# Optimization experiments

Hardware: AMD Instinct MI355X
Metric: run time of the kernel (lower is better)

The kernel has to match this reference:

```python
import jax, jax.numpy as jnp
import numpy as np
import math

N_HEAD = 12

def _tiled_causal_mask(T):
    # t x t lower-triangular mask tiled 3x3 -> T x T (T divisible by 3)
    t = T // 3
    tril = jnp.tril(jnp.ones((t, t), dtype=bool))
    return jnp.tile(tril, (3, 3))  # [T, T]

def setup_inputs() -> dict:
    key = jax.random.key(0)
    ks = jax.random.split(key, 5)
    B, T, C = 4, 1536, 768
    s = 1.0 / math.sqrt(C)
    return {
        "x": jax.random.normal(ks[0], (B, T, C), dtype=jnp.float32),
        "Wq": jax.random.normal(ks[1], (C, C), dtype=jnp.float32) * s,
        "bq": jnp.zeros((C,), dtype=jnp.float32),
        "Wk": jax.random.normal(ks[2], (C, C), dtype=jnp.float32) * s,
        "bk": jnp.zeros((C,), dtype=jnp.float32),
        "Wv": jax.random.normal(ks[3], (C, C), dtype=jnp.float32) * s,
        "bv": jnp.zeros((C,), dtype=jnp.float32),
        "Wp": jax.random.normal(ks[4], (C, C), dtype=jnp.float32) * s,
        "bp": jnp.zeros((C,), dtype=jnp.float32),
    }

def reference(x, Wq, bq, Wk, bk, Wv, bv, Wp, bp):
    B, T, C = x.shape
    H = N_HEAD
    D = C // H  # head dim
    def heads(W, b):
        return (x @ W.T + b).reshape(B, T, H, D).transpose(0, 2, 1, 3)  # [B,H,T,D]
    q = heads(Wq, bq)
    k = heads(Wk, bk)
    v = heads(Wv, bv)
    att = jnp.einsum('bhqd,bhkd->bhqk', q, k) * (1.0 / math.sqrt(D))  # [B,H,T,T]
    mask = _tiled_causal_mask(T)  # [T,T] bool
    att = jnp.where(mask[None, None], att, jnp.float32(-jnp.inf))
    att = jax.nn.softmax(att, axis=-1)
    y = jnp.einsum('bhqk,bhkd->bhqd', att, v)  # [B,H,T,D]
    y = y.transpose(0, 2, 1, 3).reshape(B, T, C)
    return y @ Wp.T + bp
```

## Files before the change

### kernel.cpp

```cpp
#include <hip/hip_runtime.h>
#include <hip/hip_bf16.h>

typedef __attribute__((ext_vector_type(8))) short bf16x8;
typedef __attribute__((ext_vector_type(4))) float f32x4;

#define NH 12
#define HD 64
#define TT 1536
#define CC 768
#define BB 4
#define MM (BB * TT)
#define LOG2E 1.44269504088896f
#define SSHIFT 14.4269504089f

__device__ __forceinline__ unsigned short f2bf(float f) {
    unsigned int u = __builtin_bit_cast(unsigned int, f);
    return (unsigned short)((u + 0x7FFFu + ((u >> 16) & 1u)) >> 16);
}

__device__ __forceinline__ unsigned short nbf(float f) {
    __hip_bfloat16 h = __float2bfloat16(f);
    return __builtin_bit_cast(unsigned short, h);
}

__device__ __forceinline__ void gl_lds16(const unsigned short* g, unsigned short* l) {
    __builtin_amdgcn_global_load_lds(
        (const __attribute__((address_space(1))) void*)g,
        (__attribute__((address_space(3))) void*)l,
        16, 0, 0);
}

#define N4W (CC * CC / 4)
#define N4X (MM * CC / 4)
__global__ __launch_bounds__(256) void convert_all(
    const float* __restrict__ x,
    const float* __restrict__ w0, const float* __restrict__ w1,
    const float* __restrict__ w2, const float* __restrict__ w3,
    unsigned short* __restrict__ xo,
    unsigned short* __restrict__ o0, unsigned short* __restrict__ o1,
    unsigned short* __restrict__ o2, unsigned short* __restrict__ o3) {
    int i = blockIdx.x * 256 + threadIdx.x;
    const float* in;
    unsigned short* out;
    int j;
    if (i < N4X) {
        in = x; out = xo; j = i;
    } else {
        int t = i - N4X;
        int which = t / N4W;
        j = t - which * N4W;
        in = which == 0 ? w0 : which == 1 ? w1 : which == 2 ? w2 : w3;
        out = which == 0 ? o0 : which == 1 ? o1 : which == 2 ? o2 : o3;
    }
    float4 v = reinterpret_cast<const float4*>(in)[j];
    ushort4 o = { f2bf(v.x), f2bf(v.y), f2bf(v.z), f2bf(v.w) };
    reinterpret_cast<ushort4*>(out)[j] = o;
}

#define GEMM_KLOOP(APTR, BPTR)                                                \
    for (int kt = 0; kt < 12; kt++) {                                         \
        const int k0 = kt * 64;                                               \
        __syncthreads();                                                      \
        _Pragma("unroll")                                                     \
        for (int i = 0; i < 4; i++) {                                         \
            gl_lds16(&APTR[(size_t)(m0 + i * 32 + sr) * CC + k0 + sc],        \
                     as0 + (i * 32 + w * 8) * 64);                            \
            gl_lds16(&BPTR[(size_t)(n0 + i * 32 + sr) * CC + k0 + sc],        \
                     bs0 + (i * 32 + w * 8) * 64);                            \
        }                                                                     \
        __syncthreads();                                                      \
        _Pragma("unroll")                                                     \
        for (int s = 0; s < 2; s++) {                                         \
            const int swz = ((s * 4 + fg) ^ (fr & 7)) * 8;                    \
            bf16x8 a[4], b[4];                                                \
            _Pragma("unroll")                                                 \
            for (int mi = 0; mi < 4; mi++)                                    \
                a[mi] = *reinterpret_cast<const bf16x8*>(                     \
                    as0 + (wr * 64 + mi * 16 + fr) * 64 + swz);               \
            _Pragma("unroll")                                                 \
            for (int ni = 0; ni < 4; ni++)                                    \
                b[ni] = *reinterpret_cast<const bf16x8*>(                     \
                    bs0 + (wc * 64 + ni * 16 + fr) * 64 + swz);               \
            _Pragma("unroll")                                                 \
            for (int mi = 0; mi < 4; mi++)                                    \
                _Pragma("unroll")                                             \
                for (int ni = 0; ni < 4; ni++)                                \
                    acc[mi][ni] = __builtin_amdgcn_mfma_f32_16x16x32_bf16(    \
                        a[mi], b[ni], acc[mi][ni], 0, 0, 0);                  \
        }                                                                     \
    }

__global__ __launch_bounds__(256) void gemm_qkv(
    const unsigned short* __restrict__ xb,
    const unsigned short* __restrict__ wq, const float* __restrict__ bq,
    const unsigned short* __restrict__ wk, const float* __restrict__ bk,
    const unsigned short* __restrict__ wv, const float* __restrict__ bv,
    unsigned short* __restrict__ qo, unsigned short* __restrict__ ko,
    unsigned short* __restrict__ vo) {
    __shared__ unsigned short As[128][64];
    __shared__ unsigned short Bs[128][64];

    const int wg = (blockIdx.x & 7) * 108 + (blockIdx.x >> 3);
    const int z = wg / 288;
    const int rem = wg % 288;
    const int m0 = (rem / 6) * 128;
    const int n0 = (rem % 6) * 128;

    const unsigned short* W = (z == 0) ? wq : (z == 1) ? wk : wv;
    const float* bias = (z == 0) ? bq : (z == 1) ? bk : bv;
    unsigned short* out = (z == 0) ? qo : (z == 1) ? ko : vo;
    const float scale = (z == 0) ? 0.125f * LOG2E : 1.0f;

    const int tid = threadIdx.x;
    const int lane = tid & 63;
    const int w = tid >> 6;
    const int wr = w >> 1, wc = w & 1;
    const int fr = lane & 15, fg = lane >> 4;

    const int sr = tid >> 3;
    const int sc = ((tid & 7) ^ ((tid >> 3) & 7)) * 8;
    unsigned short* as0 = &As[0][0];
    unsigned short* bs0 = &Bs[0][0];

    f32x4 acc[4][4];
#pragma unroll
    for (int ni = 0; ni < 4; ni++) {
        float bv_ = bias[n0 + wc * 64 + ni * 16 + fr];
#pragma unroll
        for (int mi = 0; mi < 4; mi++)
            acc[mi][ni] = (f32x4){bv_, bv_, bv_, bv_};
    }

    GEMM_KLOOP(xb, W)

#pragma unroll
    for (int mi = 0; mi < 4; mi++)
#pragma unroll
        for (int ni = 0; ni < 4; ni++) {
            int n = n0 + wc * 64 + ni * 16 + fr;
            int h = n >> 6, d = n & 63;
            int m_base = m0 + wr * 64 + mi * 16 + fg * 4;
            int b_ = m_base / TT, t0 = m_base % TT;
            if (z == 2) {
                size_t off = ((size_t)(b_ * NH + h) * HD + d) * (size_t)TT + t0;
                ushort4 o = { nbf(acc[mi][ni][0]), nbf(acc[mi][ni][1]),
                              nbf(acc[mi][ni][2]), nbf(acc[mi][ni][3]) };
                *reinterpret_cast<ushort4*>(&out[off]) = o;
            } else {
#pragma unroll
                for (int r = 0; r < 4; r++) {
                    size_t off = ((size_t)(b_ * NH + h) * TT + t0 + r) * (size_t)HD + d;
                    out[off] = nbf(acc[mi][ni][r] * scale);
                }
            }
        }
}

__global__ __launch_bounds__(256) void gemm_proj(
    const unsigned short* __restrict__ yb,
    const unsigned short* __restrict__ wp, const float* __restrict__ bp,
    float* __restrict__ out) {
    __shared__ unsigned short As[128][64];
    __shared__ unsigned short Bs[128][64];

    const int wg = (blockIdx.x & 7) * 36 + (blockIdx.x >> 3);
    const int m0 = (wg / 6) * 128;
    const int n0 = (wg % 6) * 128;

    const int tid = threadIdx.x;
    const int lane = tid & 63;
    const int w = tid >> 6;
    const int wr = w >> 1, wc = w & 1;
    const int fr = lane & 15, fg = lane >> 4;

    const int sr = tid >> 3;
    const int sc = ((tid & 7) ^ ((tid >> 3) & 7)) * 8;
    unsigned short* as0 = &As[0][0];
    unsigned short* bs0 = &Bs[0][0];

    f32x4 acc[4][4];
#pragma unroll
    for (int ni = 0; ni < 4; ni++) {
        float bv_ = bp[n0 + wc * 64 + ni * 16 + fr];
#pragma unroll
        for (int mi = 0; mi < 4; mi++)
            acc[mi][ni] = (f32x4){bv_, bv_, bv_, bv_};
    }

    GEMM_KLOOP(yb, wp)

#pragma unroll
    for (int mi = 0; mi < 4; mi++)
#pragma unroll
        for (int ni = 0; ni < 4; ni++) {
            int n = n0 + wc * 64 + ni * 16 + fr;
#pragma unroll
            for (int r = 0; r < 4; r++) {
                int m = m0 + wr * 64 + mi * 16 + fg * 4 + r;
                out[(size_t)m * CC + n] = acc[mi][ni][r];
            }
        }
}

__global__ __launch_bounds__(128, 4) void attn(
    const unsigned short* __restrict__ q, const unsigned short* __restrict__ k,
    const unsigned short* __restrict__ vt, unsigned short* __restrict__ y) {
    __shared__ unsigned short Ks[2][32][64];
    __shared__ unsigned short Vs[2][64][32];
    __shared__ unsigned short Ps[2][16][40];

    const int gid = blockIdx.x;
    const int slot = gid & 7;
    const int rest = gid >> 3;
    const int bh = slot * 6 + rest % 6;
    const int rank = rest / 6;
    const int p32 = 15 - rank / 3;
    const int sg0 = rank % 3;
    const int q0 = sg0 * 512 + p32 * 32;

    const int tid = threadIdx.x;
    const int w = tid >> 6;
    const int lane = tid & 63;
    const int fr = lane & 15, fg = lane >> 4;

    const size_t base = (size_t)bh * TT * HD;
    const unsigned short* kk = k + base;
    const unsigned short* vv = vt + base;

    bf16x8 aq[2];
#pragma unroll
    for (int s = 0; s < 2; s++)
        aq[s] = *reinterpret_cast<const bf16x8*>(
            &q[base + (size_t)(q0 + w * 16 + fr) * HD + s * 32 + fg * 8]);

    f32x4 acc_o[4];
#pragma unroll
    for (int i = 0; i < 4; i++) acc_o[i] = (f32x4){0.f, 0.f, 0.f, 0.f};
    f32x4 acc_l = (f32x4){0.f, 0.f, 0.f, 0.f};

    const bf16x8 ones8 = {(short)0x3F80, (short)0x3F80, (short)0x3F80, (short)0x3F80,
                          (short)0x3F80, (short)0x3F80, (short)0x3F80, (short)0x3F80};
    const f32x4 sinit = {-SSHIFT, -SSHIFT, -SSHIFT, -SSHIFT};

    auto stage = [&](int b, int k0n) {
#pragma unroll
        for (int i = 0; i < 2; i++) {
            const int rK = w * 16 + i * 8 + (lane >> 3);
            gl_lds16(&kk[(size_t)(k0n + rK) * HD + (((lane & 7) ^ (rK & 7)) * 8)],
                     &Ks[b][w * 16 + i * 8][0]);
            const int rV = w * 32 + i * 16 + (lane >> 2);
            gl_lds16(&vv[(size_t)rV * TT + k0n + (((lane & 3) ^ (rV & 3)) * 8)],
                     &Vs[b][w * 32 + i * 16][0]);
        }
    };

    const int per = p32 + 1;
    const int ntot = 3 * per;

    stage(0, 0);
    int cur = 0;
    int j = 0;
    int ji = 0, si = 0;
    __syncthreads();

    for (int ci = 0; ci < ntot; ci++) {
        if (ci + 1 < ntot) {
            ji++; if (ji == per) { ji = 0; si++; }
            stage(cur ^ 1, si * 512 + ji * 32);
        }

        f32x4 S[2];
#pragma unroll
        for (int nb = 0; nb < 2; nb++) {
            f32x4 sa = sinit;
            const int krow = nb * 16 + fr;
#pragma unroll
            for (int s = 0; s < 2; s++) {
                bf16x8 bk_ = *reinterpret_cast<const bf16x8*>(
                    &Ks[cur][krow][(((s * 4 + fg) ^ (krow & 7))) * 8]);
                sa = __builtin_amdgcn_mfma_f32_16x16x32_bf16(aq[s], bk_, sa, 0, 0, 0);
            }
            S[nb] = sa;
        }

        if (j == per - 1) {
#pragma unroll
            for (int nb = 0; nb < 2; nb++)
#pragma unroll
                for (int r = 0; r < 4; r++) {
                    int ib = w * 16 + fg * 4 + r;
                    int jb = nb * 16 + fr;
                    if (jb > ib) S[nb][r] = -1e30f;
                }
        }

#pragma unroll
        for (int nb = 0; nb < 2; nb++)
#pragma unroll
            for (int r = 0; r < 4; r++)
                Ps[w][fg * 4 + r][((nb ^ (fg >> 1)) * 16) + fr] =
                    nbf(exp2f(S[nb][r]));

        bf16x8 ap = *reinterpret_cast<const bf16x8*>(
            &Ps[w][fr][(fg ^ (2 * (fr >> 3))) * 8]);
#pragma unroll
        for (int nd = 0; nd < 4; nd++) {
            const int vrow = nd * 16 + fr;
            bf16x8 bv_ = *reinterpret_cast<const bf16x8*>(
                &Vs[cur][vrow][((fg ^ (vrow & 3))) * 8]);
            acc_o[nd] = __builtin_amdgcn_mfma_f32_16x16x32_bf16(ap, bv_, acc_o[nd], 0, 0, 0);
        }
        acc_l = __builtin_amdgcn_mfma_f32_16x16x32_bf16(ap, ones8, acc_l, 0, 0, 0);

        __syncthreads();
        cur ^= 1;
        if (++j == per) j = 0;
    }

    const int b_ = bh / NH, h = bh % NH;
#pragma unroll
    for (int r = 0; r < 4; r++) {
        float inv = 1.f / acc_l[r];
        int t = q0 + w * 16 + fg * 4 + r;
        size_t off = ((size_t)b_ * TT + t) * CC + h * HD;
#pragma unroll
        for (int nd = 0; nd < 4; nd++)
            y[off + nd * 16 + fr] = nbf(acc_o[nd][r] * inv);
    }
}

extern "C" void kernel_launch(void* const* d_in, const int* in_sizes, int n_in,
                              void* d_out, int out_size, void* d_ws, size_t ws_size,
                              hipStream_t stream) {
    const float* x  = (const float*)d_in[0];
    const float* Wq = (const float*)d_in[1];
    const float* bq = (const float*)d_in[2];
    const float* Wk = (const float*)d_in[3];
    const float* bk = (const float*)d_in[4];
    const float* Wv = (const float*)d_in[5];
    const float* bv = (const float*)d_in[6];
    const float* Wp = (const float*)d_in[7];
    const float* bp = (const float*)d_in[8];
    float* out = (float*)d_out;

    unsigned short* ws  = (unsigned short*)d_ws;
    unsigned short* wqb = ws;
    unsigned short* wkb = wqb + (size_t)CC * CC;
    unsigned short* wvb = wkb + (size_t)CC * CC;
    unsigned short* wpb = wvb + (size_t)CC * CC;
    unsigned short* xb  = wpb + (size_t)CC * CC;
    unsigned short* qb_ = xb  + (size_t)MM * CC;
    unsigned short* kb_ = qb_ + (size_t)MM * CC;
    unsigned short* vt_ = kb_ + (size_t)MM * CC;
    unsigned short* yb  = vt_ + (size_t)MM * CC;

    const int ntot4 = N4X + 4 * N4W;
    convert_all<<<(ntot4 + 255) / 256, 256, 0, stream>>>(
        x, Wq, Wk, Wv, Wp, xb, wqb, wkb, wvb, wpb);

    gemm_qkv<<<dim3(864), 256, 0, stream>>>(
        xb, wqb, bq, wkb, bk, wvb, bv, qb_, kb_, vt_);
    attn<<<dim3(2304), 128, 0, stream>>>(qb_, kb_, vt_, yb);
    gemm_proj<<<dim3(288), 256, 0, stream>>>(yb, wpb, bp, out);
}
```

Baseline: 112.1 us.

## Triple-buffer K/V tiles and software-pipeline QK^T one tile ahead in attention

The attention loop now keeps three K/V LDS buffers instead of two, so staging runs two tiles ahead. The QK^T MFMAs for the next tile are issued right after the exp/P write of the current tile, letting them overlap with the softmax and PV work. This is meant to hide global-to-LDS latency and MFMA dependency stalls. In exchange it uses more LDS per block and more live registers for the second S tile, which may lower occupancy under launch_bounds(128,4).

Result: slower. 120.3 us (+7.3%).

```diff
diff --git a/kernel.cpp b/kernel.cpp
--- a/kernel.cpp
+++ b/kernel.cpp
@@ -205,8 +205,8 @@
 __global__ __launch_bounds__(128, 4) void attn(
     const unsigned short* __restrict__ q, const unsigned short* __restrict__ k,
     const unsigned short* __restrict__ vt, unsigned short* __restrict__ y) {
-    __shared__ unsigned short Ks[2][32][64];
-    __shared__ unsigned short Vs[2][64][32];
+    __shared__ unsigned short Ks[3][32][64];
+    __shared__ unsigned short Vs[3][64][32];
     __shared__ unsigned short Ps[2][16][40];
 
     const int gid = blockIdx.x;
@@ -254,22 +254,7 @@
         }
     };
 
-    const int per = p32 + 1;
-    const int ntot = 3 * per;
-
-    stage(0, 0);
-    int cur = 0;
-    int j = 0;
-    int ji = 0, si = 0;
-    __syncthreads();
-
-    for (int ci = 0; ci < ntot; ci++) {
-        if (ci + 1 < ntot) {
-            ji++; if (ji == per) { ji = 0; si++; }
-            stage(cur ^ 1, si * 512 + ji * 32);
-        }
-
-        f32x4 S[2];
+    auto qk = [&](int b, bool dg, f32x4* S) {
 #pragma unroll
         for (int nb = 0; nb < 2; nb++) {
             f32x4 sa = sinit;
@@ -277,21 +262,42 @@
 #pragma unroll
             for (int s = 0; s < 2; s++) {
                 bf16x8 bk_ = *reinterpret_cast<const bf16x8*>(
-                    &Ks[cur][krow][(((s * 4 + fg) ^ (krow & 7))) * 8]);
+                    &Ks[b][krow][(((s * 4 + fg) ^ (krow & 7))) * 8]);
                 sa = __builtin_amdgcn_mfma_f32_16x16x32_bf16(aq[s], bk_, sa, 0, 0, 0);
             }
-            S[nb] = sa;
-        }
-
-        if (j == per - 1) {
-#pragma unroll
-            for (int nb = 0; nb < 2; nb++)
+            if (dg) {
 #pragma unroll
                 for (int r = 0; r < 4; r++) {
                     int ib = w * 16 + fg * 4 + r;
                     int jb = nb * 16 + fr;
-                    if (jb > ib) S[nb][r] = -1e30f;
+                    if (jb > ib) sa[r] = -1e30f;
                 }
+            }
+            S[nb] = sa;
+        }
+    };
+
+    const int per = p32 + 1;
+    const int ntot = 3 * per;
+
+    stage(0, 0);
+    int ji = 0, si = 0;
+    if (ntot > 1) {
+        ji++; if (ji == per) { ji = 0; si++; }
+        stage(1, si * 512 + ji * 32);
+    }
+    __syncthreads();
+
+    int jn = 0;
+    f32x4 S_cur[2];
+    qk(0, jn == per - 1, S_cur);
+
+    int bC = 0, bN = 1, bW = 2;
+
+    for (int ci = 0; ci < ntot; ci++) {
+        if (ci + 2 < ntot) {
+            ji++; if (ji == per) { ji = 0; si++; }
+            stage(bW, si * 512 + ji * 32);
         }
 
 #pragma unroll
@@ -299,7 +305,13 @@
 #pragma unroll
             for (int r = 0; r < 4; r++)
                 Ps[w][fg * 4 + r][((nb ^ (fg >> 1)) * 16) + fr] =
-                    nbf(exp2f(S[nb][r]));
+                    nbf(exp2f(S_cur[nb][r]));
+
+        f32x4 S_nxt[2];
+        if (ci + 1 < ntot) {
+            jn++; if (jn == per) jn = 0;
+            qk(bN, jn == per - 1, S_nxt);
+        }
 
         bf16x8 ap = *reinterpret_cast<const bf16x8*>(
             &Ps[w][fr][(fg ^ (2 * (fr >> 3))) * 8]);
@@ -307,14 +319,15 @@
         for (int nd = 0; nd < 4; nd++) {
             const int vrow = nd * 16 + fr;
             bf16x8 bv_ = *reinterpret_cast<const bf16x8*>(
-                &Vs[cur][vrow][((fg ^ (vrow & 3))) * 8]);
+                &Vs[bC][vrow][((fg ^ (vrow & 3))) * 8]);
             acc_o[nd] = __builtin_amdgcn_mfma_f32_16x16x32_bf16(ap, bv_, acc_o[nd], 0, 0, 0);
         }
         acc_l = __builtin_amdgcn_mfma_f32_16x16x32_bf16(ap, ones8, acc_l, 0, 0, 0);
 
         __syncthreads();
-        cur ^= 1;
-        if (++j == per) j = 0;
+        int t = bC; bC = bN; bN = bW; bW = t;
+        S_cur[0] = S_nxt[0];
+        S_cur[1] = S_nxt[1];
     }
 
     const int b_ = bh / NH, h = bh % NH;
```
